# Performance work log

Measured on AMD Instinct MI355X. Metric: run time of the kernel, lower is better.

The kernel has to match this reference:

```python
import jax, jax.numpy as jnp
import numpy as np

HIDDEN = 8   # TrajGRU hidden channels (hardcoded in module)
L = 5        # number of flow links
NEG = 0.2    # leaky relu slope (HKO-7 RNN_ACT_TYPE)


def conv2d(x, w, b, pad):
    y = jax.lax.conv_general_dilated(x, w, (1, 1), [(pad, pad), (pad, pad)],
                                     dimension_numbers=('NCHW', 'OIHW', 'NCHW'))
    return y + b[None, :, None, None]


def leaky(x):
    return jnp.where(x >= 0, x, NEG * x)


def bilinear_sample(im, x, y):
    # im: (C,H,W); x,y: (H,W) pixel coords; zero padding outside (grid_sample align_corners=True)
    C, H, W = im.shape
    x0 = jnp.floor(x); y0 = jnp.floor(y)
    wx = x - x0; wy = y - y0

    def g(ix, iy):
        valid = (ix >= 0) & (ix <= W - 1) & (iy >= 0) & (iy <= H - 1)
        ic = jnp.clip(ix, 0, W - 1).astype(jnp.int32)
        jc = jnp.clip(iy, 0, H - 1).astype(jnp.int32)
        return jnp.where(valid[None], im[:, jc, ic], 0.0)

    v00 = g(x0, y0); v01 = g(x0 + 1, y0)
    v10 = g(x0, y0 + 1); v11 = g(x0 + 1, y0 + 1)
    top = v00 * (1 - wx) + v01 * wx
    bot = v10 * (1 - wx) + v11 * wx
    return top * (1 - wy) + bot * wy


def trajgru_step(x, h, w_i2h, b_i2h, w_i2f, b_i2f, w_h2f, b_h2f,
                 w_flows, b_flows, w_ret, b_ret):
    B, C, H, W = h.shape
    # flow generator
    f = leaky(conv2d(x, w_i2f, b_i2f, 2) + conv2d(h, w_h2f, b_h2f, 2))
    flows = conv2d(f, w_flows, b_flows, 2).reshape(B, L, 2, H, W)
    # warp hidden along each link: wrap(h, -flow) => sample at grid - flow
    xx = jnp.arange(W, dtype=jnp.float32)[None, :] * jnp.ones((H, 1), jnp.float32)
    yy = jnp.arange(H, dtype=jnp.float32)[:, None] * jnp.ones((1, W), jnp.float32)
    cx = xx - flows[:, :, 0]  # (B,L,H,W)
    cy = yy - flows[:, :, 1]
    warp_b = jax.vmap(lambda hb, cxb, cyb:
                      jax.vmap(lambda a, b2: bilinear_sample(hb, a, b2))(cxb, cyb))
    warped = warp_b(h, cx, cy).reshape(B, L * C, H, W)  # (B, L*C, H, W)
    h2h = conv2d(warped, w_ret, b_ret, 0)
    i2h = conv2d(x, w_i2h, b_i2h, 1)
    i_r, i_u, i_m = jnp.split(i2h, 3, axis=1)
    h_r, h_u, h_m = jnp.split(h2h, 3, axis=1)
    reset = jax.nn.sigmoid(i_r + h_r)
    update = jax.nn.sigmoid(i_u + h_u)
    new_mem = leaky(i_m + reset * h_m)
    return update * h + (1.0 - update) * new_mem


def setup_inputs():
    key = jax.random.key(0)
    ks = jax.random.split(key, 16)
    B, T_in, T_out, H, W = 32, 12, 12, 128, 128
    in_ch = T_in + T_out
    p = lambda k, shape: 0.1 * jax.random.normal(k, shape, dtype=jnp.float32)
    return {
        'radar_data': jax.random.normal(ks[0], (B, T_in, 1, H, W), dtype=jnp.float32),
        'first_stage_pred': jax.random.normal(ks[1], (B, T_out, 1, H, W), dtype=jnp.float32),
        'w_conv_in': p(ks[2], (HIDDEN, in_ch, 3, 3)), 'b_conv_in': p(ks[3], (HIDDEN,)),
        'w_i2h': p(ks[4], (3 * HIDDEN, HIDDEN, 3, 3)), 'b_i2h': p(ks[5], (3 * HIDDEN,)),
        'w_i2f': p(ks[6], (32, HIDDEN, 5, 5)), 'b_i2f': p(ks[7], (32,)),
        'w_h2f': p(ks[8], (32, HIDDEN, 5, 5)), 'b_h2f': p(ks[9], (32,)),
        'w_flows': p(ks[10], (2 * L, 32, 5, 5)), 'b_flows': p(ks[11], (2 * L,)),
        'w_ret': p(ks[12], (3 * HIDDEN, L * HIDDEN, 1, 1)), 'b_ret': p(ks[13], (3 * HIDDEN,)),
        'w_conv_out': p(ks[14], (T_out, HIDDEN, 1, 1)), 'b_conv_out': p(ks[15], (T_out,)),
    }


def reference(radar_data, first_stage_pred, w_conv_in, b_conv_in, w_i2h, b_i2h,
              w_i2f, b_i2f, w_h2f, b_h2f, w_flows, b_flows, w_ret, b_ret,
              w_conv_out, b_conv_out):
    B, T_in, _, H, W = radar_data.shape
    T_out = first_stage_pred.shape[1]
    x = jnp.concatenate([radar_data.reshape(B, T_in, H, W),
                         first_stage_pred.reshape(B, T_out, H, W)], axis=1)
    x = conv2d(x, w_conv_in, b_conv_in, 1)          # (B, hidden, H, W)
    h0 = jnp.zeros((B, HIDDEN, H, W), x.dtype)       # TrajGRU zero initial state
    h = trajgru_step(x, h0, w_i2h, b_i2h, w_i2f, b_i2f, w_h2f, b_h2f,
                     w_flows, b_flows, w_ret, b_ret)  # seq_len == 1
    out = conv2d(h, w_conv_out, b_conv_out, 0)       # (B, pred_len, H, W)
    return out.reshape(B, T_out, 1, H, W)
```

## Files before the change

### kernel.cpp

```cpp
#include <hip/hip_runtime.h>
#include <hip/hip_bf16.h>


typedef __fp16   h2f __attribute__((ext_vector_type(2)));
typedef _Float16 v8h __attribute__((ext_vector_type(8)));
typedef float    v4f __attribute__((ext_vector_type(4)));

#define HW 128
#define SPITCH 24

#define WB_HOFF 4608
#define FLT_OFF 16384
#define N_PREP  7828

__global__ __launch_bounds__(256)
void prep(const float* __restrict__ w_in,  const float* __restrict__ b_in,
          const float* __restrict__ w_i2h, const float* __restrict__ b_i2h,
          const float* __restrict__ b_ret, const float* __restrict__ w_out,
          const float* __restrict__ b_out, void* __restrict__ ws)
{
    int idx = blockIdx.x * 256 + threadIdx.x;
    _Float16* wh = (_Float16*)ws;
    float* fw = (float*)((char*)ws + FLT_OFF);
    if (idx < 4608) {
        int j = idx & 7, r = idx >> 3;
        int lane = r & 63, sg = r >> 6;
        int g = sg % 3, s = sg / 3;
        int quad = lane >> 4, n = lane & 15;
        int tap = s * 4 + quad;
        float v = (n < 8 && tap < 9) ? w_in[n*216 + (g*8 + j)*9 + tap] : 0.f;
        wh[idx] = (_Float16)v;
    } else if (idx < 7680) {
        int i2 = idx - 4608;
        int j = i2 & 7, r = i2 >> 3;
        int lane = r & 63; r >>= 6;
        int nt = r & 1, s = r >> 1;
        int quad = lane >> 4, n = lane & 15;
        int kk = s * 32 + quad * 8 + j;
        int t = kk >> 3, m = kk & 7;
        int o = nt * 16 + n;
        float v = (t < 9 && o < 24) ? w_i2h[o*72 + m*9 + t] : 0.f;
        wh[WB_HOFF + i2] = (_Float16)v;
    } else if (idx < N_PREP) {
        int j = idx - 7680;
        float v;
        if (j < 32) {
            int c = j & 7, sel = j >> 3;
            v = (sel==0) ? b_i2h[c]    + b_ret[c]
              : (sel==1) ? b_i2h[8+c]  + b_ret[8+c]
              : (sel==2) ? b_i2h[16+c] : b_ret[16+c];
        } else if (j < 128) v = w_out[j-32];
        else if (j < 140)   v = b_out[j-128];
        else                v = b_in[j-140];
        fw[j] = v;
    }
}

__device__ __forceinline__ void pack_store(_Float16* dst, const float* v)
{
    union { h2f h2[12]; v8h h8[3]; } u;
#pragma unroll
    for (int k = 0; k < 12; ++k)
        u.h2[k] = __builtin_amdgcn_cvt_pkrtz(v[2 * k], v[2 * k + 1]);
#pragma unroll
    for (int k = 0; k < 3; ++k) *(v8h*)&dst[8 * k] = u.h8[k];
}

__global__ __launch_bounds__(256, 8)
void radar2_mfma(const float* __restrict__ radar,
                 const float* __restrict__ pred,
                 const void*  __restrict__ ws,
                 float* __restrict__ out)
{
    __shared__ __align__(16) char pool[400 * SPITCH * 2];
    _Float16* s_in = (_Float16*)pool;
    _Float16* s_x  = (_Float16*)pool;
    float*    s_hc = (float*)(pool + 5376);

    const _Float16* wh = (const _Float16*)ws;
    const float* fw = (const float*)((const char*)ws + FLT_OFF);

    const int tid  = threadIdx.x;
    const int lane = tid & 63;
    const int wave = tid >> 6;
    const int quad = lane >> 4;
    const int col  = lane & 15;

    const int id   = blockIdx.x;
    const int b    = (id & 7) * 4 + ((id >> 3) >> 6);
    const int tile = (id >> 3) & 63;
    const int ty0  = (tile >> 3) << 4;
    const int tx0  = (tile & 7) << 4;

    const float* rb = radar + (((size_t)b * 12) << 14);
    const float* pb = pred  + (((size_t)b * 12) << 14);

    const int r0 = tid, r1 = tid + 256;
    const int ly0 = r0 / 20, lx0 = r0 - 20 * ly0;
    const int gy0 = ty0 + ly0 - 2, gx0 = tx0 + lx0 - 2;
    const bool in0 = ((unsigned)gy0 < HW) & ((unsigned)gx0 < HW);
    const int off0 = (gy0 << 7) + gx0;
    const bool has1 = (r1 < 400);
    const int ly1 = r1 / 20, lx1 = r1 - 20 * ly1;
    const int gy1 = ty0 + ly1 - 2, gx1 = tx0 + lx1 - 2;
    const bool in1 = has1 & ((unsigned)gy1 < HW) & ((unsigned)gx1 < HW);
    const int off1 = (gy1 << 7) + gx1;

    float va[24], vb24[24];
#pragma unroll
    for (int c = 0; c < 12; ++c) {
        va[c]      = in0 ? rb[((size_t)c << 14) + off0] : 0.f;
        va[12 + c] = in0 ? pb[((size_t)c << 14) + off0] : 0.f;
    }
#pragma unroll
    for (int c = 0; c < 12; ++c) {
        vb24[c]      = in1 ? rb[((size_t)c << 14) + off1] : 0.f;
        vb24[12 + c] = in1 ? pb[((size_t)c << 14) + off1] : 0.f;
    }
    pack_store(&s_in[r0 * SPITCH], va);
    if (has1) pack_store(&s_in[r1 * SPITCH], vb24);

    v8h bfA[9];
#pragma unroll
    for (int i = 0; i < 9; ++i) bfA[i] = *(const v8h*)&wh[(i * 64 + lane) * 8];
    __syncthreads();

    int toffA[3];
#pragma unroll
    for (int s = 0; s < 3; ++s) {
        int t = s * 4 + quad;
        toffA[s] = (t < 9) ? ((t / 3) * 20 + (t % 3)) * SPITCH : 0;
    }
    int pbase[6];
#pragma unroll
    for (int t = 0; t < 6; ++t) {
        int p = (wave + 4 * t) * 16 + col; if (p > 323) p = 323;
        pbase[t] = ((p / 18) * 20 + (p % 18)) * SPITCH;
    }
    v4f accA[6];
#pragma unroll
    for (int t = 0; t < 6; ++t) accA[t] = (v4f){0.f, 0.f, 0.f, 0.f};
#pragma unroll
    for (int t = 0; t < 6; ++t) {
        if (wave + 4 * t < 21) {
#pragma unroll
            for (int s = 0; s < 3; ++s) {
                int ab = pbase[t] + toffA[s];
#pragma unroll
                for (int g = 0; g < 3; ++g) {
                    v8h a = *(const v8h*)&s_in[ab + g * 8];
                    accA[t] = __builtin_amdgcn_mfma_f32_16x16x32_f16(a, bfA[s * 3 + g], accA[t], 0, 0, 0);
                }
            }
        }
    }
    __syncthreads();

    const float binv = fw[140 + (col & 7)];
    if (col < 8) {
#pragma unroll
        for (int t = 0; t < 6; ++t) {
            int mt = wave + 4 * t;
            if (mt < 21) {
#pragma unroll
                for (int r = 0; r < 4; ++r) {
                    int pa = mt * 16 + quad * 4 + r;
                    int py = pa / 18, px = pa - 18 * py;
                    bool ok = (pa < 324) &&
                              ((unsigned)(ty0 + py - 1) < HW) &&
                              ((unsigned)(tx0 + px - 1) < HW);
                    s_x[pa * 8 + col] = (_Float16)(ok ? accA[t][r] + binv : 0.f);
                }
            }
        }
    }
    __syncthreads();

    int toff2[3];
#pragma unroll
    for (int s = 0; s < 3; ++s) {
        int t = s * 4 + quad;
        toff2[s] = (t < 9) ? ((t / 3) * 18 + (t % 3)) * 8 : 0;
    }
    v8h bfB[3][2];
#pragma unroll
    for (int s = 0; s < 3; ++s)
#pragma unroll
        for (int nt = 0; nt < 2; ++nt)
            bfB[s][nt] = *(const v8h*)&wh[WB_HOFF + ((s * 2 + nt) * 64 + lane) * 8];

    v4f acc0[4], acc1[4];
#pragma unroll
    for (int t = 0; t < 4; ++t) {
        acc0[t] = (v4f){0.f, 0.f, 0.f, 0.f};
        acc1[t] = (v4f){0.f, 0.f, 0.f, 0.f};
    }
#pragma unroll
    for (int t = 0; t < 4; ++t) {
        int abase = ((wave + 4 * t) * 18 + col) * 8;
#pragma unroll
        for (int s = 0; s < 3; ++s) {
            v8h a = *(const v8h*)&s_x[abase + toff2[s]];
            acc0[t] = __builtin_amdgcn_mfma_f32_16x16x32_f16(a, bfB[s][0], acc0[t], 0, 0, 0);
            acc1[t] = __builtin_amdgcn_mfma_f32_16x16x32_f16(a, bfB[s][1], acc1[t], 0, 0, 0);
        }
    }

    const int c7 = lane & 7;
    const float g0v = fw[c7], g1v = fw[8 + c7], g2v = fw[16 + c7], g3v = fw[24 + c7];
#pragma unroll
    for (int t = 0; t < 4; ++t) {
        int mt = wave + 4 * t;
#pragma unroll
        for (int r = 0; r < 4; ++r) {
            float iu = __shfl_xor(acc0[t][r], 8, 64);
            if (col < 8) {
                float rr = 1.f / (1.f + __expf(-(acc0[t][r] + g0v)));
                float uu = 1.f / (1.f + __expf(-(iu + g1v)));
                float mm = acc1[t][r] + g2v + rr * g3v;
                mm = (mm >= 0.f) ? mm : 0.2f * mm;
                s_hc[(mt * 16 + quad * 4 + r) * 9 + c7] = (1.f - uu) * mm;
            }
        }
    }
    __syncthreads();

    float h[8];
#pragma unroll
    for (int c = 0; c < 8; ++c) h[c] = s_hc[tid * 9 + c];
    const float* wout = fw + 32;
    const float* bout = fw + 128;
    const int oy = tid >> 4, ox = tid & 15;
    float* op = out + (((size_t)b * 12) << 14) + ((ty0 + oy) << 7) + (tx0 + ox);
#pragma unroll
    for (int t = 0; t < 12; ++t) {
        float o = bout[t];
#pragma unroll
        for (int c = 0; c < 8; ++c) o = fmaf(h[c], wout[t * 8 + c], o);
        op[(size_t)t << 14] = o;
    }
}

extern "C" void kernel_launch(void* const* d_in, const int* in_sizes, int n_in,
                              void* d_out, int out_size, void* d_ws, size_t ws_size,
                              hipStream_t stream) {
    (void)in_sizes; (void)n_in; (void)ws_size; (void)out_size;
    const float* radar = (const float*)d_in[0];
    const float* pred  = (const float*)d_in[1];
    const float* w_in  = (const float*)d_in[2];
    const float* b_in  = (const float*)d_in[3];
    const float* w_i2h = (const float*)d_in[4];
    const float* b_i2h = (const float*)d_in[5];
    const float* b_ret = (const float*)d_in[13];
    const float* w_out = (const float*)d_in[14];
    const float* b_out = (const float*)d_in[15];

    prep<<<(N_PREP + 255) / 256, 256, 0, stream>>>(w_in, b_in, w_i2h, b_i2h,
                                                   b_ret, w_out, b_out, d_ws);

    radar2_mfma<<<dim3(2048), dim3(256), 0, stream>>>(radar, pred, d_ws, (float*)d_out);
}
```

Baseline: 167.3 us.

## Widen tiles to 16x32 with 512-thread blocks to cut halo overhead

```diff
diff --git a/kernel.cpp b/kernel.cpp
--- a/kernel.cpp
+++ b/kernel.cpp
@@ -8,6 +8,10 @@
 
 #define HW 128
 #define SPITCH 24
+#define PCOLS 36
+#define NPOS  720
+#define SXW   34
+#define SXN   612
 
 #define WB_HOFF 4608
 #define FLT_OFF 16384
@@ -66,16 +70,16 @@
     for (int k = 0; k < 3; ++k) *(v8h*)&dst[8 * k] = u.h8[k];
 }
 
-__global__ __launch_bounds__(256, 8)
+__global__ __launch_bounds__(512, 8)
 void radar2_mfma(const float* __restrict__ radar,
                  const float* __restrict__ pred,
                  const void*  __restrict__ ws,
                  float* __restrict__ out)
 {
-    __shared__ __align__(16) char pool[400 * SPITCH * 2];
+    __shared__ __align__(16) char pool[NPOS * SPITCH * 2];
     _Float16* s_in = (_Float16*)pool;
     _Float16* s_x  = (_Float16*)pool;
-    float*    s_hc = (float*)(pool + 5376);
+    float*    s_hc = (float*)(pool + 9792);
 
     const _Float16* wh = (const _Float16*)ws;
     const float* fw = (const float*)((const char*)ws + FLT_OFF);
@@ -87,21 +91,21 @@
     const int col  = lane & 15;
 
     const int id   = blockIdx.x;
-    const int b    = (id & 7) * 4 + ((id >> 3) >> 6);
-    const int tile = (id >> 3) & 63;
-    const int ty0  = (tile >> 3) << 4;
-    const int tx0  = (tile & 7) << 4;
+    const int b    = (id & 7) * 4 + (id >> 8);
+    const int tile = (id >> 3) & 31;
+    const int ty0  = (tile >> 2) << 4;
+    const int tx0  = (tile & 3) << 5;
 
     const float* rb = radar + (((size_t)b * 12) << 14);
     const float* pb = pred  + (((size_t)b * 12) << 14);
 
-    const int r0 = tid, r1 = tid + 256;
-    const int ly0 = r0 / 20, lx0 = r0 - 20 * ly0;
+    const int r0 = tid, r1 = tid + 512;
+    const int ly0 = r0 / PCOLS, lx0 = r0 - PCOLS * ly0;
     const int gy0 = ty0 + ly0 - 2, gx0 = tx0 + lx0 - 2;
     const bool in0 = ((unsigned)gy0 < HW) & ((unsigned)gx0 < HW);
     const int off0 = (gy0 << 7) + gx0;
-    const bool has1 = (r1 < 400);
-    const int ly1 = r1 / 20, lx1 = r1 - 20 * ly1;
+    const bool has1 = (r1 < NPOS);
+    const int ly1 = r1 / PCOLS, lx1 = r1 - PCOLS * ly1;
     const int gy1 = ty0 + ly1 - 2, gx1 = tx0 + lx1 - 2;
     const bool in1 = has1 & ((unsigned)gy1 < HW) & ((unsigned)gx1 < HW);
     const int off1 = (gy1 << 7) + gx1;
@@ -119,37 +123,37 @@
     }
     pack_store(&s_in[r0 * SPITCH], va);
     if (has1) pack_store(&s_in[r1 * SPITCH], vb24);
-
-    v8h bfA[9];
-#pragma unroll
-    for (int i = 0; i < 9; ++i) bfA[i] = *(const v8h*)&wh[(i * 64 + lane) * 8];
     __syncthreads();
 
     int toffA[3];
 #pragma unroll
     for (int s = 0; s < 3; ++s) {
         int t = s * 4 + quad;
-        toffA[s] = (t < 9) ? ((t / 3) * 20 + (t % 3)) * SPITCH : 0;
-    }
-    int pbase[6];
-#pragma unroll
-    for (int t = 0; t < 6; ++t) {
-        int p = (wave + 4 * t) * 16 + col; if (p > 323) p = 323;
-        pbase[t] = ((p / 18) * 20 + (p % 18)) * SPITCH;
-    }
-    v4f accA[6];
-#pragma unroll
-    for (int t = 0; t < 6; ++t) accA[t] = (v4f){0.f, 0.f, 0.f, 0.f};
-#pragma unroll
-    for (int t = 0; t < 6; ++t) {
-        if (wave + 4 * t < 21) {
-#pragma unroll
-            for (int s = 0; s < 3; ++s) {
+        toffA[s] = (t < 9) ? ((t / 3) * PCOLS + (t % 3)) * SPITCH : 0;
+    }
+    int pbase[5];
+#pragma unroll
+    for (int t = 0; t < 5; ++t) {
+        int p = (wave + 8 * t) * 16 + col; if (p > SXN - 1) p = SXN - 1;
+        pbase[t] = ((p / SXW) * PCOLS + (p % SXW)) * SPITCH;
+    }
+    v4f accA[5];
+#pragma unroll
+    for (int t = 0; t < 5; ++t) accA[t] = (v4f){0.f, 0.f, 0.f, 0.f};
+#pragma unroll
+    for (int s = 0; s < 3; ++s) {
+        v8h bg[3];
+#pragma unroll
+        for (int g = 0; g < 3; ++g)
+            bg[g] = *(const v8h*)&wh[((s * 3 + g) * 64 + lane) * 8];
+#pragma unroll
+        for (int t = 0; t < 5; ++t) {
+            if (wave + 8 * t < 39) {
                 int ab = pbase[t] + toffA[s];
 #pragma unroll
                 for (int g = 0; g < 3; ++g) {
                     v8h a = *(const v8h*)&s_in[ab + g * 8];
-                    accA[t] = __builtin_amdgcn_mfma_f32_16x16x32_f16(a, bfA[s * 3 + g], accA[t], 0, 0, 0);
+                    accA[t] = __builtin_amdgcn_mfma_f32_16x16x32_f16(a, bg[g], accA[t], 0, 0, 0);
                 }
             }
         }
@@ -159,17 +163,17 @@
     const float binv = fw[140 + (col & 7)];
     if (col < 8) {
 #pragma unroll
-        for (int t = 0; t < 6; ++t) {
-            int mt = wave + 4 * t;
-            if (mt < 21) {
+        for (int t = 0; t < 5; ++t) {
+            int mt = wave + 8 * t;
+            if (mt < 39) {
 #pragma unroll
                 for (int r = 0; r < 4; ++r) {
                     int pa = mt * 16 + quad * 4 + r;
-                    int py = pa / 18, px = pa - 18 * py;
-                    bool ok = (pa < 324) &&
-                              ((unsigned)(ty0 + py - 1) < HW) &&
+                    int py = pa / SXW, px = pa - SXW * py;
+                    bool ok = ((unsigned)(ty0 + py - 1) < HW) &&
                               ((unsigned)(tx0 + px - 1) < HW);
-                    s_x[pa * 8 + col] = (_Float16)(ok ? accA[t][r] + binv : 0.f);
+                    if (pa < SXN)
+                        s_x[pa * 8 + col] = (_Float16)(ok ? accA[t][r] + binv : 0.f);
                 }
             }
         }
@@ -180,15 +184,14 @@
 #pragma unroll
     for (int s = 0; s < 3; ++s) {
         int t = s * 4 + quad;
-        toff2[s] = (t < 9) ? ((t / 3) * 18 + (t % 3)) * 8 : 0;
-    }
-    v8h bfB[3][2];
-#pragma unroll
-    for (int s = 0; s < 3; ++s)
-#pragma unroll
-        for (int nt = 0; nt < 2; ++nt)
-            bfB[s][nt] = *(const v8h*)&wh[WB_HOFF + ((s * 2 + nt) * 64 + lane) * 8];
-
+        toff2[s] = (t < 9) ? ((t / 3) * SXW + (t % 3)) * 8 : 0;
+    }
+    int abase2[4];
+#pragma unroll
+    for (int t = 0; t < 4; ++t) {
+        int q = (wave + 8 * t) * 16 + col;
+        abase2[t] = ((q >> 5) * SXW + (q & 31)) * 8;
+    }
     v4f acc0[4], acc1[4];
 #pragma unroll
     for (int t = 0; t < 4; ++t) {
@@ -196,13 +199,14 @@
         acc1[t] = (v4f){0.f, 0.f, 0.f, 0.f};
     }
 #pragma unroll
-    for (int t = 0; t < 4; ++t) {
-        int abase = ((wave + 4 * t) * 18 + col) * 8;
-#pragma unroll
-        for (int s = 0; s < 3; ++s) {
-            v8h a = *(const v8h*)&s_x[abase + toff2[s]];
-            acc0[t] = __builtin_amdgcn_mfma_f32_16x16x32_f16(a, bfB[s][0], acc0[t], 0, 0, 0);
-            acc1[t] = __builtin_amdgcn_mfma_f32_16x16x32_f16(a, bfB[s][1], acc1[t], 0, 0, 0);
+    for (int s = 0; s < 3; ++s) {
+        v8h b0 = *(const v8h*)&wh[WB_HOFF + ((s * 2 + 0) * 64 + lane) * 8];
+        v8h b1 = *(const v8h*)&wh[WB_HOFF + ((s * 2 + 1) * 64 + lane) * 8];
+#pragma unroll
+        for (int t = 0; t < 4; ++t) {
+            v8h a = *(const v8h*)&s_x[abase2[t] + toff2[s]];
+            acc0[t] = __builtin_amdgcn_mfma_f32_16x16x32_f16(a, b0, acc0[t], 0, 0, 0);
+            acc1[t] = __builtin_amdgcn_mfma_f32_16x16x32_f16(a, b1, acc1[t], 0, 0, 0);
         }
     }
 
@@ -210,7 +214,7 @@
     const float g0v = fw[c7], g1v = fw[8 + c7], g2v = fw[16 + c7], g3v = fw[24 + c7];
 #pragma unroll
     for (int t = 0; t < 4; ++t) {
-        int mt = wave + 4 * t;
+        int mt = wave + 8 * t;
 #pragma unroll
         for (int r = 0; r < 4; ++r) {
             float iu = __shfl_xor(acc0[t][r], 8, 64);
@@ -230,7 +234,7 @@
     for (int c = 0; c < 8; ++c) h[c] = s_hc[tid * 9 + c];
     const float* wout = fw + 32;
     const float* bout = fw + 128;
-    const int oy = tid >> 4, ox = tid & 15;
+    const int oy = tid >> 5, ox = tid & 31;
     float* op = out + (((size_t)b * 12) << 14) + ((ty0 + oy) << 7) + (tx0 + ox);
 #pragma unroll
     for (int t = 0; t < 12; ++t) {
@@ -258,5 +262,5 @@
     prep<<<(N_PREP + 255) / 256, 256, 0, stream>>>(w_in, b_in, w_i2h, b_i2h,
                                                    b_ret, w_out, b_out, d_ws);
 
-    radar2_mfma<<<dim3(2048), dim3(256), 0, stream>>>(radar, pred, d_ws, (float*)d_out);
-}
+    radar2_mfma<<<dim3(1024), dim3(512), 0, stream>>>(radar, pred, d_ws, (float*)d_out);
+}
```

Result: faster. 140.5 us (-16.0%).
